# Kernel optimization log

Measured on AMD Instinct MI355X. Metric: run time of the kernel, lower is better.

The kernel has to match this reference:

```python
import jax, jax.numpy as jnp
import numpy as np

D = 768      # hidden size (hardcoded in module)
H = 8        # MHA heads
DH = D // H  # head dim = 96
SLOPE = 0.01 # LeakyReLU default negative slope
NEG = -1e9


def _leaky(x):
    return jnp.where(x >= 0, x, SLOPE * x)


def setup_inputs() -> dict:
    key = jax.random.key(0)
    ks = jax.random.split(key, 20)
    B, S, T, C, L = 32, 2048, 64, 512, 16
    seq = jax.random.normal(ks[0], (B, S, D), dtype=jnp.float32)
    tab_ids = jax.random.randint(ks[1], (B, T, L), 0, S, dtype=jnp.int32)
    col_ids = jax.random.randint(ks[2], (B, C, L), 0, S, dtype=jnp.int32)
    # contiguous column->table assignment (8 cols/table), mirrors cumulative
    # slicing by column_number_in_each_table and keeps every table non-empty
    t_of_c = jnp.broadcast_to(jnp.repeat(jnp.arange(T, dtype=jnp.int32), C // T), (B, C))
    g = lambda k, sh: (jax.random.normal(k, sh, dtype=jnp.float32) * 0.02)
    return {
        "sequence_embeddings": seq,
        "table_token_ids": tab_ids,
        "column_token_ids": col_ids,
        "table_of_column": t_of_c,
        "W_tab_pool": g(ks[3], (D, D)), "b_tab_pool": g(ks[4], (D,)),
        "W_col_pool": g(ks[5], (D, D)), "b_col_pool": g(ks[6], (D,)),
        "in_proj_w": g(ks[7], (3 * D, D)), "in_proj_b": g(ks[8], (3 * D,)),
        "out_proj_w": g(ks[9], (D, D)), "out_proj_b": g(ks[10], (D,)),
        "W_t1": g(ks[11], (D, 256)), "b_t1": g(ks[12], (256,)),
        "W_t2": g(ks[13], (256, 2)), "b_t2": g(ks[14], (2,)),
        "W_c1": g(ks[15], (D, 256)), "b_c1": g(ks[16], (256,)),
        "W_c2": g(ks[17], (256, 2)), "b_c2": g(ks[18], (2,)),
    }


def reference(sequence_embeddings, table_token_ids, column_token_ids, table_of_column,
              W_tab_pool, b_tab_pool, W_col_pool, b_col_pool,
              in_proj_w, in_proj_b, out_proj_w, out_proj_b,
              W_t1, b_t1, W_t2, b_t2, W_c1, b_c1, W_c2, b_c2):
    B, T = table_token_ids.shape[:2]
    C = column_token_ids.shape[1]
    bi = jnp.arange(B)[:, None, None]
    # ragged span sum-pooling (gather + segment sum)
    tab = sequence_embeddings[bi, table_token_ids].sum(axis=2)   # [B,T,D]
    col = sequence_embeddings[bi, column_token_ids].sum(axis=2)  # [B,C,D]
    tab = _leaky(tab @ W_tab_pool + b_tab_pool)
    col = _leaky(col @ W_col_pool + b_col_pool)
    # per-table cross-attention (table query over its own columns), batched + masked
    Wq, Wk, Wv = jnp.split(in_proj_w, 3, axis=0)
    bq, bk, bv = jnp.split(in_proj_b, 3, axis=0)
    q = (tab @ Wq.T + bq).reshape(B, T, H, DH)
    k = (col @ Wk.T + bk).reshape(B, C, H, DH)
    v = (col @ Wv.T + bv).reshape(B, C, H, DH)
    scores = jnp.einsum('bthd,bchd->bhtc', q, k) / jnp.sqrt(jnp.float32(DH))
    mask = table_of_column[:, None, None, :] == jnp.arange(T, dtype=table_of_column.dtype)[None, None, :, None]
    attn = jax.nn.softmax(jnp.where(mask, scores, NEG), axis=-1)
    ctx = jnp.einsum('bhtc,bchd->bthd', attn, v).reshape(B, T, D)
    tab = tab + (ctx @ out_proj_w.T + out_proj_b)
    tab = tab / jnp.maximum(jnp.linalg.norm(tab, axis=-1, keepdims=True), 1e-12)
    # classification heads (dropout in eval mode = identity)
    t_logits = _leaky(tab @ W_t1 + b_t1) @ W_t2 + b_t2  # [B,T,2]
    c_logits = _leaky(col @ W_c1 + b_c1) @ W_c2 + b_c2  # [B,C,2]
    return jnp.concatenate([t_logits, c_logits], axis=1)  # [B,T+C,2]
```

## Files before the change

kernel.cpp:

```cpp
#include <hip/hip_runtime.h>
#include <hip/hip_bf16.h>

constexpr int Bc = 32;
constexpr int Sc = 2048;
constexpr int Tc = 64;
constexpr int Cc = 512;
constexpr int Lc = 16;
constexpr int Dc = 768;
constexpr int Hc = 8;
constexpr int DHc = 96;

typedef __attribute__((ext_vector_type(4))) float f32x4;
typedef __attribute__((ext_vector_type(8))) short bf16x8;
typedef __hip_bfloat16 bf;

__device__ inline unsigned short f2bf(float f) {
  __hip_bfloat16 h = __float2bfloat16(f);
  return *reinterpret_cast<unsigned short*>(&h);
}
__device__ inline float us2f(unsigned short u) {
  return __uint_as_float(((unsigned)u) << 16);
}

#define GLDS16(gp, lp)                                                        \
  __builtin_amdgcn_global_load_lds(                                           \
      (const __attribute__((address_space(1))) void*)(gp),                    \
      (__attribute__((address_space(3))) void*)(lp), 16, 0, 0)

__device__ inline void transpose32(const float* __restrict__ in,
                                   bf* __restrict__ outp, int K, int N,
                                   int ti, float (*t)[33]) {
  int nx = N >> 5;
  int bx = (ti % nx) * 32, by = (ti / nx) * 32;
  int x = threadIdx.x & 31, y = threadIdx.x >> 5;
#pragma unroll
  for (int i = 0; i < 32; i += 8)
    t[y + i][x] = in[(size_t)(by + y + i) * N + bx + x];
  __syncthreads();
#pragma unroll
  for (int i = 0; i < 32; i += 8)
    outp[(size_t)(bx + y + i) * K + by + x] = __float2bfloat16(t[x][y + i]);
}

__global__ __launch_bounds__(256) void prep_kernel(
    const float* __restrict__ W_tab_pool, const float* __restrict__ W_col_pool,
    const float* __restrict__ W_t1, const float* __restrict__ W_c1,
    const float* __restrict__ in_proj_w, const float* __restrict__ out_proj_w,
    const float* __restrict__ b_t2, const float* __restrict__ b_c2,
    const float* __restrict__ seq, const int* __restrict__ t_of_c,
    bf* __restrict__ wtab_t, bf* __restrict__ wcol_t, bf* __restrict__ wt1_t,
    bf* __restrict__ wc1_t, bf* __restrict__ winproj, bf* __restrict__ woutproj,
    float* __restrict__ outd, ushort* __restrict__ seqb,
    int* __restrict__ col_sorted, int* __restrict__ offs) {
  __shared__ float t[32][33];
  __shared__ int cnt[Tc];
  __shared__ int cur[Tc + 1];
  int blk = blockIdx.x, tid = threadIdx.x;
  if (blk < 576) {
    transpose32(W_tab_pool, wtab_t, Dc, Dc, blk, t);
  } else if (blk < 1152) {
    transpose32(W_col_pool, wcol_t, Dc, Dc, blk - 576, t);
  } else if (blk < 1344) {
    transpose32(W_t1, wt1_t, Dc, 256, blk - 1152, t);
  } else if (blk < 1536) {
    transpose32(W_c1, wc1_t, Dc, 256, blk - 1344, t);
  } else if (blk < 3264) {
    int i = (blk - 1536) * 256 + tid;
    float4 v = reinterpret_cast<const float4*>(in_proj_w)[i];
    reinterpret_cast<ushort4*>(winproj)[i] =
        make_ushort4(f2bf(v.x), f2bf(v.y), f2bf(v.z), f2bf(v.w));
  } else if (blk < 3840) {
    int i = (blk - 3264) * 256 + tid;
    float4 v = reinterpret_cast<const float4*>(out_proj_w)[i];
    reinterpret_cast<ushort4*>(woutproj)[i] =
        make_ushort4(f2bf(v.x), f2bf(v.y), f2bf(v.z), f2bf(v.w));
  } else if (blk < 3984) {
    int e = (blk - 3840) * 256 + tid;
    int i = e & 1;
    int r = (e >> 1) % (Tc + Cc);
    outd[e] = (r < Tc) ? b_t2[i] : b_c2[i];
  } else if (blk < 28560) {
    int i0 = (blk - 3984) * 512 + tid;
    const float4* s4 = reinterpret_cast<const float4*>(seq);
    ushort4* o4 = reinterpret_cast<ushort4*>(seqb);
    float4 v = s4[i0];
    o4[i0] = make_ushort4(f2bf(v.x), f2bf(v.y), f2bf(v.z), f2bf(v.w));
    float4 v2 = s4[i0 + 256];
    o4[i0 + 256] = make_ushort4(f2bf(v2.x), f2bf(v2.y), f2bf(v2.z), f2bf(v2.w));
  } else {
    int b = blk - 28560;
    if (tid < Tc) cnt[tid] = 0;
    __syncthreads();
    for (int c = tid; c < Cc; c += 256) atomicAdd(&cnt[t_of_c[b * Cc + c]], 1);
    __syncthreads();
    if (tid == 0) {
      int off = 0;
      for (int tt = 0; tt < Tc; ++tt) {
        cur[tt] = off;
        off += cnt[tt];
      }
      cur[Tc] = off;
    }
    __syncthreads();
    if (tid <= Tc) offs[b * (Tc + 1) + tid] = cur[tid];
    __syncthreads();
    for (int c = tid; c < Cc; c += 256) {
      int tt = t_of_c[b * Cc + c];
      int pos = atomicAdd(&cur[tt], 1);
      col_sorted[b * Cc + pos] = c;
    }
  }
}

__global__ __launch_bounds__(256) void pool_kernel(
    const ushort* __restrict__ seqb, const int* __restrict__ tab_ids,
    const int* __restrict__ col_ids, ushort* __restrict__ tabp,
    ushort* __restrict__ colp) {
  int swz = (blockIdx.x & 7) * 576 + (blockIdx.x >> 3);
  int w = threadIdx.x >> 6, l = threadIdx.x & 63;
  int row = swz * 4 + w;
  int b = row / (Tc + Cc), r = row % (Tc + Cc);
  const int* ids;
  ushort* outp;
  if (r < Tc) {
    ids = tab_ids + ((size_t)b * Tc + r) * Lc;
    outp = tabp + ((size_t)b * Tc + r) * Dc;
  } else {
    int c = r - Tc;
    ids = col_ids + ((size_t)b * Cc + c) * Lc;
    outp = colp + ((size_t)b * Cc + c) * Dc;
  }
  float a0[4] = {0, 0, 0, 0}, a1[4] = {0, 0, 0, 0}, a2[4] = {0, 0, 0, 0};
#pragma unroll
  for (int tix = 0; tix < Lc; ++tix) {
    const ushort4* p =
        reinterpret_cast<const ushort4*>(seqb + ((size_t)b * Sc + ids[tix]) * Dc);
    ushort4 u0 = p[l], u1 = p[l + 64], u2 = p[l + 128];
    a0[0] += us2f(u0.x); a0[1] += us2f(u0.y); a0[2] += us2f(u0.z); a0[3] += us2f(u0.w);
    a1[0] += us2f(u1.x); a1[1] += us2f(u1.y); a1[2] += us2f(u1.z); a1[3] += us2f(u1.w);
    a2[0] += us2f(u2.x); a2[1] += us2f(u2.y); a2[2] += us2f(u2.z); a2[3] += us2f(u2.w);
  }
  ushort4* ob = reinterpret_cast<ushort4*>(outp);
  ob[l] = make_ushort4(f2bf(a0[0]), f2bf(a0[1]), f2bf(a0[2]), f2bf(a0[3]));
  ob[l + 64] = make_ushort4(f2bf(a1[0]), f2bf(a1[1]), f2bf(a1[2]), f2bf(a1[3]));
  ob[l + 128] = make_ushort4(f2bf(a2[0]), f2bf(a2[1]), f2bf(a2[2]), f2bf(a2[3]));
}

__device__ __forceinline__ void gemm_core(
    const bf* __restrict__ A, const bf* __restrict__ Bt,
    const float* __restrict__ bias, bf* __restrict__ Obf,
    float* __restrict__ Of32, const float* __restrict__ w2,
    float* __restrict__ outd, int out_base, int log2rpb, int bx, int by, int N,
    int leaky, int outmode) {
  constexpr int BM = 128, BN = 128, BK = 64, K = Dc;
  __shared__ bf As[BM * BK];
  __shared__ bf Bs[BN * BK];
  int tid = threadIdx.x;
  int row0 = by * BM, col0 = bx * BN;
  int w = tid >> 6, l = tid & 63;
  int wr = (w >> 1) * 64, wc = (w & 1) * 64;
  f32x4 acc[4][4];
#pragma unroll
  for (int m = 0; m < 4; ++m)
#pragma unroll
    for (int n = 0; n < 4; ++n) acc[m][n] = f32x4{0.f, 0.f, 0.f, 0.f};

  int srow = tid >> 3, skk = (tid & 7) * 8;
  const bf* gA = A + (size_t)(row0 + srow) * K + skk;
  const bf* gB = Bt + (size_t)(col0 + srow) * K + skk;
  char* lA = (char*)As + tid * 16;
  char* lB = (char*)Bs + tid * 16;
  int lr = l & 15, lk = (l >> 4) * 8;

  for (int k0 = 0; k0 < K; k0 += BK) {
#pragma unroll
    for (int c = 0; c < 4; ++c) {
      GLDS16(gA + k0 + (size_t)c * 32 * K, lA + c * 4096);
      GLDS16(gB + k0 + (size_t)c * 32 * K, lB + c * 4096);
    }
    __syncthreads();
    bf16x8 af[2][4], bfr[2][4];
#pragma unroll
    for (int ks = 0; ks < 2; ++ks) {
#pragma unroll
      for (int m = 0; m < 4; ++m)
        af[ks][m] = *reinterpret_cast<const bf16x8*>(
            &As[(wr + m * 16 + lr) * BK + ks * 32 + lk]);
#pragma unroll
      for (int n = 0; n < 4; ++n)
        bfr[ks][n] = *reinterpret_cast<const bf16x8*>(
            &Bs[(wc + n * 16 + lr) * BK + ks * 32 + lk]);
    }
#pragma unroll
    for (int ks = 0; ks < 2; ++ks)
#pragma unroll
      for (int m = 0; m < 4; ++m)
#pragma unroll
        for (int n = 0; n < 4; ++n)
          acc[m][n] = __builtin_amdgcn_mfma_f32_16x16x32_bf16(
              af[ks][m], bfr[ks][n], acc[m][n], 0, 0, 0);
    __syncthreads();
  }

  int colI = l & 15, rowb = (l >> 4) * 4;
  if (outmode == 3) {
    float w20[4], w21[4], bv[4];
#pragma unroll
    for (int n = 0; n < 4; ++n) {
      int c = col0 + wc + n * 16 + colI;
      w20[n] = w2[c * 2];
      w21[n] = w2[c * 2 + 1];
      bv[n] = bias[c];
    }
    float p0[4][4], p1[4][4];
#pragma unroll
    for (int m = 0; m < 4; ++m)
#pragma unroll
      for (int j = 0; j < 4; ++j) { p0[m][j] = 0.f; p1[m][j] = 0.f; }
#pragma unroll
    for (int m = 0; m < 4; ++m)
#pragma unroll
      for (int n = 0; n < 4; ++n)
#pragma unroll
        for (int j = 0; j < 4; ++j) {
          float v = acc[m][n][j] + bv[n];
          v = v >= 0.f ? v : 0.01f * v;
          p0[m][j] += v * w20[n];
          p1[m][j] += v * w21[n];
        }
#pragma unroll
    for (int m = 0; m < 4; ++m)
#pragma unroll
      for (int j = 0; j < 4; ++j) {
#pragma unroll
        for (int msk = 1; msk <= 8; msk <<= 1) {
          p0[m][j] += __shfl_xor(p0[m][j], msk);
          p1[m][j] += __shfl_xor(p1[m][j], msk);
        }
      }
    if (colI == 0) {
#pragma unroll
      for (int m = 0; m < 4; ++m)
#pragma unroll
        for (int j = 0; j < 4; ++j) {
          int grow = row0 + wr + m * 16 + rowb + j;
          int bb = grow >> log2rpb;
          int rr = grow & ((1 << log2rpb) - 1);
          int orow = bb * (Tc + Cc) + out_base + rr;
          atomicAdd(&outd[(size_t)orow * 2], p0[m][j]);
          atomicAdd(&outd[(size_t)orow * 2 + 1], p1[m][j]);
        }
    }
    return;
  }
#pragma unroll
  for (int m = 0; m < 4; ++m) {
#pragma unroll
    for (int n = 0; n < 4; ++n) {
      int c = col0 + wc + n * 16 + colI;
      float bv = bias ? bias[c] : 0.f;
#pragma unroll
      for (int j = 0; j < 4; ++j) {
        int r = row0 + wr + m * 16 + rowb + j;
        float v = acc[m][n][j] + bv;
        if (leaky) v = v >= 0.f ? v : 0.01f * v;
        if (outmode == 0 || outmode == 2) Obf[(size_t)r * N + c] = __float2bfloat16(v);
        if (outmode == 1 || outmode == 2) Of32[(size_t)r * N + c] = v;
      }
    }
  }
}

__global__ __launch_bounds__(256) void gemm_pools(
    const bf* __restrict__ tabp, const bf* __restrict__ colp,
    const bf* __restrict__ wtab_t, const bf* __restrict__ wcol_t,
    const float* __restrict__ b_tab, const float* __restrict__ b_col,
    bf* __restrict__ tabb_bf, float* __restrict__ tabb_f,
    bf* __restrict__ colb) {
  int id = (blockIdx.x & 7) * 108 + (blockIdx.x >> 3);
  if (id < 96) {
    gemm_core(tabp, wtab_t, b_tab, tabb_bf, tabb_f, nullptr, nullptr, 0, 0,
              id % 6, id / 6, Dc, 1, 2);
  } else {
    int r = id - 96;
    gemm_core(colp, wcol_t, b_col, colb, nullptr, nullptr, nullptr, 0, 0,
              r % 6, r / 6, Dc, 1, 0);
  }
}

__global__ __launch_bounds__(256) void gemm_qkvc(
    const bf* __restrict__ tabb_bf, const bf* __restrict__ colb,
    const bf* __restrict__ winproj, const float* __restrict__ in_proj_b,
    const bf* __restrict__ wc1_t, const float* __restrict__ b_c1,
    const float* __restrict__ W_c2, bf* __restrict__ qb, bf* __restrict__ kvb,
    float* __restrict__ outd) {
  int id = (blockIdx.x & 7) * 236 + (blockIdx.x >> 3);
  if (id < 96) {
    gemm_core(tabb_bf, winproj, in_proj_b, qb, nullptr, nullptr, nullptr, 0, 0,
              id % 6, id / 6, Dc, 0, 0);
  } else if (id < 1632) {
    int r = id - 96;
    gemm_core(colb, winproj + (size_t)Dc * Dc, in_proj_b + Dc, kvb, nullptr,
              nullptr, nullptr, 0, 0, r % 12, r / 12, 1536, 0, 0);
  } else {
    int r = id - 1632;
    gemm_core(colb, wc1_t, b_c1, nullptr, nullptr, W_c2, outd, Tc, 9, r % 2,
              r / 2, 256, 1, 3);
  }
}

__global__ __launch_bounds__(256) void gemm_single(
    const bf* __restrict__ A, const bf* __restrict__ Bt,
    const float* __restrict__ bias, bf* __restrict__ Obf,
    float* __restrict__ Of32, const float* __restrict__ w2,
    float* __restrict__ outd, int out_base, int log2rpb, int nbx, int N,
    int leaky, int outmode) {
  int chunk = gridDim.x >> 3;
  int id = (blockIdx.x & 7) * chunk + (blockIdx.x >> 3);
  gemm_core(A, Bt, bias, Obf, Of32, w2, outd, out_base, log2rpb, id % nbx,
            id / nbx, N, leaky, outmode);
}

__global__ __launch_bounds__(256) void attn_kernel(
    const bf* __restrict__ q, const bf* __restrict__ kv,
    const int* __restrict__ col_sorted, const int* __restrict__ offs,
    bf* __restrict__ ctx) {
  int b = blockIdx.x / Tc;
  int t = blockIdx.x % Tc;
  __shared__ float pbuf[Hc][Cc];
  __shared__ float den[Hc];
  __shared__ int cols_s[Cc];
  int tid = threadIdx.x;
  int o0 = offs[b * (Tc + 1) + t];
  int n = offs[b * (Tc + 1) + t + 1] - o0;
  for (int i = tid; i < n; i += 256)
    cols_s[i] = col_sorted[(size_t)b * Cc + o0 + i];
  __syncthreads();
  int h = tid >> 5, l32 = tid & 31, g = l32 >> 3, i8 = l32 & 7;
  const float scale = 0.10206207261596577f;
  float q12[12];
  {
    const ushort* qp =
        (const ushort*)q + ((size_t)b * Tc + t) * Dc + h * DHc + i8 * 12;
    ushort4 u0 = *(const ushort4*)(qp);
    ushort4 u1 = *(const ushort4*)(qp + 4);
    ushort4 u2 = *(const ushort4*)(qp + 8);
    q12[0] = us2f(u0.x); q12[1] = us2f(u0.y); q12[2] = us2f(u0.z); q12[3] = us2f(u0.w);
    q12[4] = us2f(u1.x); q12[5] = us2f(u1.y); q12[6] = us2f(u1.z); q12[7] = us2f(u1.w);
    q12[8] = us2f(u2.x); q12[9] = us2f(u2.y); q12[10] = us2f(u2.z); q12[11] = us2f(u2.w);
  }
  if (n > 0) {
    for (int jb = 0; jb < n; jb += 4) {
      int j = jb + g;
      float s = 0.f;
      if (j < n) {
        const ushort* kp = (const ushort*)kv +
                           ((size_t)b * Cc + cols_s[j]) * 1536 + h * DHc + i8 * 12;
        ushort4 u0 = *(const ushort4*)(kp);
        ushort4 u1 = *(const ushort4*)(kp + 4);
        ushort4 u2 = *(const ushort4*)(kp + 8);
        s += q12[0] * us2f(u0.x) + q12[1] * us2f(u0.y) + q12[2] * us2f(u0.z) +
             q12[3] * us2f(u0.w);
        s += q12[4] * us2f(u1.x) + q12[5] * us2f(u1.y) + q12[6] * us2f(u1.z) +
             q12[7] * us2f(u1.w);
        s += q12[8] * us2f(u2.x) + q12[9] * us2f(u2.y) + q12[10] * us2f(u2.z) +
             q12[11] * us2f(u2.w);
      }
      s += __shfl_xor(s, 1);
      s += __shfl_xor(s, 2);
      s += __shfl_xor(s, 4);
      if (j < n && i8 == 0) pbuf[h][j] = s * scale;
    }
  }
  __syncthreads();
  if (n > 0) {
    float lmax = -3.0e38f;
    for (int j = l32; j < n; j += 32) lmax = fmaxf(lmax, pbuf[h][j]);
#pragma unroll
    for (int m = 16; m >= 1; m >>= 1) lmax = fmaxf(lmax, __shfl_xor(lmax, m));
    float lsum = 0.f;
    for (int j = l32; j < n; j += 32) {
      float e = __expf(pbuf[h][j] - lmax);
      pbuf[h][j] = e;
      lsum += e;
    }
#pragma unroll
    for (int m = 16; m >= 1; m >>= 1) lsum += __shfl_xor(lsum, m);
    if (l32 == 0) den[h] = lsum;
  } else if (l32 == 0) {
    den[h] = (float)Cc;
  }
  __syncthreads();
  int ncols = n > 0 ? n : Cc;
  float a12[12];
#pragma unroll
  for (int d = 0; d < 12; ++d) a12[d] = 0.f;
  for (int jb = 0; jb < ncols; jb += 4) {
    int j = jb + g;
    if (j < ncols) {
      int cj = n > 0 ? cols_s[j] : j;
      float pw = n > 0 ? pbuf[h][j] : 1.f;
      const ushort* vp = (const ushort*)kv + ((size_t)b * Cc + cj) * 1536 +
                         768 + h * DHc + i8 * 12;
      ushort4 u0 = *(const ushort4*)(vp);
      ushort4 u1 = *(const ushort4*)(vp + 4);
      ushort4 u2 = *(const ushort4*)(vp + 8);
      a12[0] += pw * us2f(u0.x); a12[1] += pw * us2f(u0.y);
      a12[2] += pw * us2f(u0.z); a12[3] += pw * us2f(u0.w);
      a12[4] += pw * us2f(u1.x); a12[5] += pw * us2f(u1.y);
      a12[6] += pw * us2f(u1.z); a12[7] += pw * us2f(u1.w);
      a12[8] += pw * us2f(u2.x); a12[9] += pw * us2f(u2.y);
      a12[10] += pw * us2f(u2.z); a12[11] += pw * us2f(u2.w);
    }
  }
#pragma unroll
  for (int d = 0; d < 12; ++d) {
    a12[d] += __shfl_xor(a12[d], 8);
    a12[d] += __shfl_xor(a12[d], 16);
  }
  float inv = 1.0f / den[h];
  if (g == 0) {
    ushort* cp = (ushort*)ctx + ((size_t)b * Tc + t) * Dc + h * DHc + i8 * 12;
    *(ushort4*)(cp) = make_ushort4(f2bf(a12[0] * inv), f2bf(a12[1] * inv),
                                   f2bf(a12[2] * inv), f2bf(a12[3] * inv));
    *(ushort4*)(cp + 4) = make_ushort4(f2bf(a12[4] * inv), f2bf(a12[5] * inv),
                                       f2bf(a12[6] * inv), f2bf(a12[7] * inv));
    *(ushort4*)(cp + 8) = make_ushort4(f2bf(a12[8] * inv), f2bf(a12[9] * inv),
                                       f2bf(a12[10] * inv), f2bf(a12[11] * inv));
  }
}

__global__ __launch_bounds__(256) void addnorm_kernel(
    const float* __restrict__ tab, const float* __restrict__ proj,
    bf* __restrict__ tabn) {
  int row = blockIdx.x;
  int tid = threadIdx.x;
  size_t base = (size_t)row * Dc;
  float x0 = tab[base + tid] + proj[base + tid];
  float x1 = tab[base + tid + 256] + proj[base + tid + 256];
  float x2 = tab[base + tid + 512] + proj[base + tid + 512];
  float ss = x0 * x0 + x1 * x1 + x2 * x2;
#pragma unroll
  for (int m = 32; m >= 1; m >>= 1) ss += __shfl_xor(ss, m);
  __shared__ float red[4];
  int wave = tid >> 6, lane = tid & 63;
  if (lane == 0) red[wave] = ss;
  __syncthreads();
  float total = red[0] + red[1] + red[2] + red[3];
  float sc = 1.0f / fmaxf(sqrtf(total), 1e-12f);
  tabn[base + tid] = __float2bfloat16(x0 * sc);
  tabn[base + tid + 256] = __float2bfloat16(x1 * sc);
  tabn[base + tid + 512] = __float2bfloat16(x2 * sc);
}

extern "C" void kernel_launch(void* const* d_in, const int* in_sizes, int n_in,
                              void* d_out, int out_size, void* d_ws,
                              size_t ws_size, hipStream_t stream) {
  const float* seq = (const float*)d_in[0];
  const int* tab_ids = (const int*)d_in[1];
  const int* col_ids = (const int*)d_in[2];
  const int* t_of_c = (const int*)d_in[3];
  const float* W_tab_pool = (const float*)d_in[4];
  const float* b_tab_pool = (const float*)d_in[5];
  const float* W_col_pool = (const float*)d_in[6];
  const float* b_col_pool = (const float*)d_in[7];
  const float* in_proj_w = (const float*)d_in[8];
  const float* in_proj_b = (const float*)d_in[9];
  const float* out_proj_w = (const float*)d_in[10];
  const float* out_proj_b = (const float*)d_in[11];
  const float* W_t1 = (const float*)d_in[12];
  const float* b_t1 = (const float*)d_in[13];
  const float* W_t2 = (const float*)d_in[14];
  const float* b_t2 = (const float*)d_in[15];
  const float* W_c1 = (const float*)d_in[16];
  const float* b_c1 = (const float*)d_in[17];
  const float* W_c2 = (const float*)d_in[18];
  const float* b_c2 = (const float*)d_in[19];
  float* out = (float*)d_out;

  char* p = (char*)d_ws;
  auto alloc = [&](size_t bytes) -> char* {
    char* r = p;
    p += (bytes + 255) & ~(size_t)255;
    return r;
  };
  const size_t nBT = (size_t)Bc * Tc;
  const size_t nBC = (size_t)Bc * Cc;
  ushort* seqb = (ushort*)alloc((size_t)Bc * Sc * Dc * 2);
  bf* tabp = (bf*)alloc(nBT * Dc * 2);
  bf* colp = (bf*)alloc(nBC * Dc * 2);
  bf* tabb_bf = (bf*)alloc(nBT * Dc * 2);
  float* tabb_f = (float*)alloc(nBT * Dc * 4);
  bf* colb = (bf*)alloc(nBC * Dc * 2);
  bf* qb = (bf*)alloc(nBT * Dc * 2);
  bf* kvb = (bf*)alloc(nBC * 1536 * 2);
  bf* ctxb = (bf*)alloc(nBT * Dc * 2);
  float* projb = (float*)alloc(nBT * Dc * 4);
  bf* tabn = (bf*)alloc(nBT * Dc * 2);
  bf* wtab_t = (bf*)alloc((size_t)Dc * Dc * 2);
  bf* wcol_t = (bf*)alloc((size_t)Dc * Dc * 2);
  bf* winproj = (bf*)alloc((size_t)3 * Dc * Dc * 2);
  bf* woutproj = (bf*)alloc((size_t)Dc * Dc * 2);
  bf* wt1_t = (bf*)alloc((size_t)256 * Dc * 2);
  bf* wc1_t = (bf*)alloc((size_t)256 * Dc * 2);
  int* col_sorted = (int*)alloc(nBC * 4);
  int* offs = (int*)alloc((size_t)Bc * (Tc + 1) * 4);

  prep_kernel<<<28592, 256, 0, stream>>>(
      W_tab_pool, W_col_pool, W_t1, W_c1, in_proj_w, out_proj_w, b_t2, b_c2,
      seq, t_of_c, wtab_t, wcol_t, wt1_t, wc1_t, winproj, woutproj, out,
      seqb, col_sorted, offs);
  pool_kernel<<<Bc * (Tc + Cc) / 4, 256, 0, stream>>>(seqb, tab_ids, col_ids,
                                                      (ushort*)tabp,
                                                      (ushort*)colp);
  gemm_pools<<<864, 256, 0, stream>>>(tabp, colp, wtab_t, wcol_t, b_tab_pool,
                                      b_col_pool, tabb_bf, tabb_f, colb);
  gemm_qkvc<<<1888, 256, 0, stream>>>(tabb_bf, colb, winproj, in_proj_b, wc1_t,
                                      b_c1, W_c2, qb, kvb, out);
  attn_kernel<<<Bc * Tc, 256, 0, stream>>>(qb, kvb, col_sorted, offs, ctxb);
  gemm_single<<<96, 256, 0, stream>>>(ctxb, woutproj, out_proj_b, nullptr,
                                      projb, nullptr, nullptr, 0, 0, 6, Dc, 0,
                                      1);
  addnorm_kernel<<<nBT, 256, 0, stream>>>(tabb_f, projb, tabn);
  gemm_single<<<32, 256, 0, stream>>>(tabn, wt1_t, b_t1, nullptr, nullptr,
                                      W_t2, out, 0, 6, 2, 256, 1, 3);
}
```

Measured before the change: 572.1 us.

## Double-buffer GEMM LDS, fuse residual+norm into out-proj epilogue, rebalance kernels

The shared GEMM core now uses double-buffered LDS tiles, so the next K slice is prefetched while the current one feeds the MFMA instructions, and one barrier per iteration is dropped. The separate add-and-normalize kernel is removed. The out-projection epilogue now adds the residual, writes bf16, and accumulates per-row sums of squares with atomics. The final t1 head applies the 1/norm scale inside its epilogue. The column classification head moves from the QKV launch into the out-projection launch, which removes one launch and one fp32 round trip, at the cost of doubled LDS per block (lower occupancy) and atomic-order nondeterminism.

```diff
diff --git a/kernel.cpp b/kernel.cpp
--- a/kernel.cpp
+++ b/kernel.cpp
@@ -51,7 +51,8 @@
     bf* __restrict__ wtab_t, bf* __restrict__ wcol_t, bf* __restrict__ wt1_t,
     bf* __restrict__ wc1_t, bf* __restrict__ winproj, bf* __restrict__ woutproj,
     float* __restrict__ outd, ushort* __restrict__ seqb,
-    int* __restrict__ col_sorted, int* __restrict__ offs) {
+    int* __restrict__ col_sorted, int* __restrict__ offs,
+    float* __restrict__ ssq) {
   __shared__ float t[32][33];
   __shared__ int cnt[Tc];
   __shared__ int cur[Tc + 1];
@@ -87,7 +88,7 @@
     o4[i0] = make_ushort4(f2bf(v.x), f2bf(v.y), f2bf(v.z), f2bf(v.w));
     float4 v2 = s4[i0 + 256];
     o4[i0 + 256] = make_ushort4(f2bf(v2.x), f2bf(v2.y), f2bf(v2.z), f2bf(v2.w));
-  } else {
+  } else if (blk < 28592) {
     int b = blk - 28560;
     if (tid < Tc) cnt[tid] = 0;
     __syncthreads();
@@ -109,6 +110,9 @@
       int pos = atomicAdd(&cur[tt], 1);
       col_sorted[b * Cc + pos] = c;
     }
+  } else {
+#pragma unroll
+    for (int i = 0; i < 8; ++i) ssq[tid * 8 + i] = 0.f;
   }
 }
 
@@ -150,11 +154,13 @@
     const bf* __restrict__ A, const bf* __restrict__ Bt,
     const float* __restrict__ bias, bf* __restrict__ Obf,
     float* __restrict__ Of32, const float* __restrict__ w2,
-    float* __restrict__ outd, int out_base, int log2rpb, int bx, int by, int N,
-    int leaky, int outmode) {
+    float* __restrict__ outd, int out_base, int log2rpb,
+    const float* __restrict__ tabf, float* __restrict__ ssq,
+    const float* __restrict__ ssrd, int bx, int by, int N, int leaky,
+    int outmode) {
   constexpr int BM = 128, BN = 128, BK = 64, K = Dc;
-  __shared__ bf As[BM * BK];
-  __shared__ bf Bs[BN * BK];
+  __shared__ bf As[2][BM * BK];
+  __shared__ bf Bs[2][BN * BK];
   int tid = threadIdx.x;
   int row0 = by * BM, col0 = bx * BN;
   int w = tid >> 6, l = tid & 63;
@@ -168,28 +174,37 @@
   int srow = tid >> 3, skk = (tid & 7) * 8;
   const bf* gA = A + (size_t)(row0 + srow) * K + skk;
   const bf* gB = Bt + (size_t)(col0 + srow) * K + skk;
-  char* lA = (char*)As + tid * 16;
-  char* lB = (char*)Bs + tid * 16;
+  char* lA = (char*)&As[0][0] + tid * 16;
+  char* lB = (char*)&Bs[0][0] + tid * 16;
   int lr = l & 15, lk = (l >> 4) * 8;
 
+#pragma unroll
+  for (int c = 0; c < 4; ++c) {
+    GLDS16(gA + (size_t)c * 32 * K, lA + c * 4096);
+    GLDS16(gB + (size_t)c * 32 * K, lB + c * 4096);
+  }
+  __syncthreads();
+  int cur = 0;
   for (int k0 = 0; k0 < K; k0 += BK) {
-#pragma unroll
-    for (int c = 0; c < 4; ++c) {
-      GLDS16(gA + k0 + (size_t)c * 32 * K, lA + c * 4096);
-      GLDS16(gB + k0 + (size_t)c * 32 * K, lB + c * 4096);
-    }
-    __syncthreads();
+    if (k0 + BK < K) {
+      int nb = cur ^ 1;
+#pragma unroll
+      for (int c = 0; c < 4; ++c) {
+        GLDS16(gA + k0 + BK + (size_t)c * 32 * K, lA + nb * 16384 + c * 4096);
+        GLDS16(gB + k0 + BK + (size_t)c * 32 * K, lB + nb * 16384 + c * 4096);
+      }
+    }
     bf16x8 af[2][4], bfr[2][4];
 #pragma unroll
     for (int ks = 0; ks < 2; ++ks) {
 #pragma unroll
       for (int m = 0; m < 4; ++m)
         af[ks][m] = *reinterpret_cast<const bf16x8*>(
-            &As[(wr + m * 16 + lr) * BK + ks * 32 + lk]);
+            &As[cur][(wr + m * 16 + lr) * BK + ks * 32 + lk]);
 #pragma unroll
       for (int n = 0; n < 4; ++n)
         bfr[ks][n] = *reinterpret_cast<const bf16x8*>(
-            &Bs[(wc + n * 16 + lr) * BK + ks * 32 + lk]);
+            &Bs[cur][(wc + n * 16 + lr) * BK + ks * 32 + lk]);
     }
 #pragma unroll
     for (int ks = 0; ks < 2; ++ks)
@@ -199,7 +214,8 @@
         for (int n = 0; n < 4; ++n)
           acc[m][n] = __builtin_amdgcn_mfma_f32_16x16x32_bf16(
               af[ks][m], bfr[ks][n], acc[m][n], 0, 0, 0);
-    __syncthreads();
+    if (k0 + BK < K) __syncthreads();
+    cur ^= 1;
   }
 
   int colI = l & 15, rowb = (l >> 4) * 4;
@@ -212,6 +228,18 @@
       w21[n] = w2[c * 2 + 1];
       bv[n] = bias[c];
     }
+    float scr[4][4];
+#pragma unroll
+    for (int m = 0; m < 4; ++m)
+#pragma unroll
+      for (int j = 0; j < 4; ++j) {
+        if (ssrd) {
+          int r = row0 + wr + m * 16 + rowb + j;
+          scr[m][j] = 1.f / fmaxf(sqrtf(ssrd[r]), 1e-12f);
+        } else {
+          scr[m][j] = 1.f;
+        }
+      }
     float p0[4][4], p1[4][4];
 #pragma unroll
     for (int m = 0; m < 4; ++m)
@@ -223,7 +251,7 @@
       for (int n = 0; n < 4; ++n)
 #pragma unroll
         for (int j = 0; j < 4; ++j) {
-          float v = acc[m][n][j] + bv[n];
+          float v = scr[m][j] * acc[m][n][j] + bv[n];
           v = v >= 0.f ? v : 0.01f * v;
           p0[m][j] += v * w20[n];
           p1[m][j] += v * w21[n];
@@ -253,6 +281,43 @@
     }
     return;
   }
+  if (outmode == 4) {
+    float sq[4][4];
+#pragma unroll
+    for (int m = 0; m < 4; ++m)
+#pragma unroll
+      for (int j = 0; j < 4; ++j) sq[m][j] = 0.f;
+#pragma unroll
+    for (int m = 0; m < 4; ++m)
+#pragma unroll
+      for (int n = 0; n < 4; ++n) {
+        int c = col0 + wc + n * 16 + colI;
+        float bv = bias[c];
+#pragma unroll
+        for (int j = 0; j < 4; ++j) {
+          int r = row0 + wr + m * 16 + rowb + j;
+          float x = acc[m][n][j] + bv + tabf[(size_t)r * N + c];
+          Obf[(size_t)r * N + c] = __float2bfloat16(x);
+          sq[m][j] += x * x;
+        }
+      }
+#pragma unroll
+    for (int m = 0; m < 4; ++m)
+#pragma unroll
+      for (int j = 0; j < 4; ++j) {
+#pragma unroll
+        for (int msk = 1; msk <= 8; msk <<= 1)
+          sq[m][j] += __shfl_xor(sq[m][j], msk);
+      }
+    if (colI == 0) {
+#pragma unroll
+      for (int m = 0; m < 4; ++m)
+#pragma unroll
+        for (int j = 0; j < 4; ++j)
+          atomicAdd(&ssq[row0 + wr + m * 16 + rowb + j], sq[m][j]);
+    }
+    return;
+  }
 #pragma unroll
   for (int m = 0; m < 4; ++m) {
 #pragma unroll
@@ -264,8 +329,8 @@
         int r = row0 + wr + m * 16 + rowb + j;
         float v = acc[m][n][j] + bv;
         if (leaky) v = v >= 0.f ? v : 0.01f * v;
-        if (outmode == 0 || outmode == 2) Obf[(size_t)r * N + c] = __float2bfloat16(v);
-        if (outmode == 1 || outmode == 2) Of32[(size_t)r * N + c] = v;
+        Obf[(size_t)r * N + c] = __float2bfloat16(v);
+        if (outmode == 2 && Of32) Of32[(size_t)r * N + c] = v;
       }
     }
   }
@@ -278,47 +343,63 @@
     bf* __restrict__ tabb_bf, float* __restrict__ tabb_f,
     bf* __restrict__ colb) {
   int id = (blockIdx.x & 7) * 108 + (blockIdx.x >> 3);
+  const bf* Aa; const bf* Bb; const float* bb; bf* Oo; float* Ff;
+  int bx, by;
   if (id < 96) {
-    gemm_core(tabp, wtab_t, b_tab, tabb_bf, tabb_f, nullptr, nullptr, 0, 0,
-              id % 6, id / 6, Dc, 1, 2);
+    Aa = tabp; Bb = wtab_t; bb = b_tab; Oo = tabb_bf; Ff = tabb_f;
+    bx = id % 6; by = id / 6;
   } else {
     int r = id - 96;
-    gemm_core(colp, wcol_t, b_col, colb, nullptr, nullptr, nullptr, 0, 0,
-              r % 6, r / 6, Dc, 1, 0);
-  }
-}
-
-__global__ __launch_bounds__(256) void gemm_qkvc(
+    Aa = colp; Bb = wcol_t; bb = b_col; Oo = colb; Ff = nullptr;
+    bx = r % 6; by = r / 6;
+  }
+  gemm_core(Aa, Bb, bb, Oo, Ff, nullptr, nullptr, 0, 0, nullptr, nullptr,
+            nullptr, bx, by, Dc, 1, 2);
+}
+
+__global__ __launch_bounds__(256) void gemm_qkv(
     const bf* __restrict__ tabb_bf, const bf* __restrict__ colb,
     const bf* __restrict__ winproj, const float* __restrict__ in_proj_b,
+    bf* __restrict__ qb, bf* __restrict__ kvb) {
+  int id = (blockIdx.x & 7) * 204 + (blockIdx.x >> 3);
+  const bf* Aa; const bf* Bb; const float* bb; bf* Oo;
+  int bx, by, NN;
+  if (id < 96) {
+    Aa = tabb_bf; Bb = winproj; bb = in_proj_b; Oo = qb;
+    bx = id % 6; by = id / 6; NN = Dc;
+  } else {
+    int r = id - 96;
+    Aa = colb; Bb = winproj + (size_t)Dc * Dc; bb = in_proj_b + Dc; Oo = kvb;
+    bx = r % 12; by = r / 12; NN = 1536;
+  }
+  gemm_core(Aa, Bb, bb, Oo, nullptr, nullptr, nullptr, 0, 0, nullptr, nullptr,
+            nullptr, bx, by, NN, 0, 0);
+}
+
+__global__ __launch_bounds__(256) void gemm_oc(
+    const bf* __restrict__ ctxb, const bf* __restrict__ woutproj,
+    const float* __restrict__ out_proj_b, const float* __restrict__ tabb_f,
+    bf* __restrict__ xbf, float* __restrict__ ssq, const bf* __restrict__ colb,
     const bf* __restrict__ wc1_t, const float* __restrict__ b_c1,
-    const float* __restrict__ W_c2, bf* __restrict__ qb, bf* __restrict__ kvb,
-    float* __restrict__ outd) {
-  int id = (blockIdx.x & 7) * 236 + (blockIdx.x >> 3);
+    const float* __restrict__ W_c2, float* __restrict__ outd) {
+  int id = (blockIdx.x & 7) * 44 + (blockIdx.x >> 3);
   if (id < 96) {
-    gemm_core(tabb_bf, winproj, in_proj_b, qb, nullptr, nullptr, nullptr, 0, 0,
-              id % 6, id / 6, Dc, 0, 0);
-  } else if (id < 1632) {
+    gemm_core(ctxb, woutproj, out_proj_b, xbf, nullptr, nullptr, nullptr, 0, 0,
+              tabb_f, ssq, nullptr, id % 6, id / 6, Dc, 0, 4);
+  } else {
     int r = id - 96;
-    gemm_core(colb, winproj + (size_t)Dc * Dc, in_proj_b + Dc, kvb, nullptr,
-              nullptr, nullptr, 0, 0, r % 12, r / 12, 1536, 0, 0);
-  } else {
-    int r = id - 1632;
-    gemm_core(colb, wc1_t, b_c1, nullptr, nullptr, W_c2, outd, Tc, 9, r % 2,
-              r / 2, 256, 1, 3);
-  }
-}
-
-__global__ __launch_bounds__(256) void gemm_single(
-    const bf* __restrict__ A, const bf* __restrict__ Bt,
-    const float* __restrict__ bias, bf* __restrict__ Obf,
-    float* __restrict__ Of32, const float* __restrict__ w2,
-    float* __restrict__ outd, int out_base, int log2rpb, int nbx, int N,
-    int leaky, int outmode) {
-  int chunk = gridDim.x >> 3;
-  int id = (blockIdx.x & 7) * chunk + (blockIdx.x >> 3);
-  gemm_core(A, Bt, bias, Obf, Of32, w2, outd, out_base, log2rpb, id % nbx,
-            id / nbx, N, leaky, outmode);
+    gemm_core(colb, wc1_t, b_c1, nullptr, nullptr, W_c2, outd, Tc, 9, nullptr,
+              nullptr, nullptr, r % 2, r / 2, 256, 1, 3);
+  }
+}
+
+__global__ __launch_bounds__(256) void gemm_t1(
+    const bf* __restrict__ xbf, const bf* __restrict__ wt1_t,
+    const float* __restrict__ b_t1, const float* __restrict__ W_t2,
+    const float* __restrict__ ssq, float* __restrict__ outd) {
+  int id = (blockIdx.x & 7) * 4 + (blockIdx.x >> 3);
+  gemm_core(xbf, wt1_t, b_t1, nullptr, nullptr, W_t2, outd, 0, 6, nullptr,
+            nullptr, ssq, id % 2, id / 2, 256, 1, 3);
 }
 
 __global__ __launch_bounds__(256) void attn_kernel(
@@ -430,29 +511,6 @@
   }
 }
 
-__global__ __launch_bounds__(256) void addnorm_kernel(
-    const float* __restrict__ tab, const float* __restrict__ proj,
-    bf* __restrict__ tabn) {
-  int row = blockIdx.x;
-  int tid = threadIdx.x;
-  size_t base = (size_t)row * Dc;
-  float x0 = tab[base + tid] + proj[base + tid];
-  float x1 = tab[base + tid + 256] + proj[base + tid + 256];
-  float x2 = tab[base + tid + 512] + proj[base + tid + 512];
-  float ss = x0 * x0 + x1 * x1 + x2 * x2;
-#pragma unroll
-  for (int m = 32; m >= 1; m >>= 1) ss += __shfl_xor(ss, m);
-  __shared__ float red[4];
-  int wave = tid >> 6, lane = tid & 63;
-  if (lane == 0) red[wave] = ss;
-  __syncthreads();
-  float total = red[0] + red[1] + red[2] + red[3];
-  float sc = 1.0f / fmaxf(sqrtf(total), 1e-12f);
-  tabn[base + tid] = __float2bfloat16(x0 * sc);
-  tabn[base + tid + 256] = __float2bfloat16(x1 * sc);
-  tabn[base + tid + 512] = __float2bfloat16(x2 * sc);
-}
-
 extern "C" void kernel_launch(void* const* d_in, const int* in_sizes, int n_in,
                               void* d_out, int out_size, void* d_ws,
                               size_t ws_size, hipStream_t stream) {
@@ -495,8 +553,8 @@
   bf* qb = (bf*)alloc(nBT * Dc * 2);
   bf* kvb = (bf*)alloc(nBC * 1536 * 2);
   bf* ctxb = (bf*)alloc(nBT * Dc * 2);
-  float* projb = (float*)alloc(nBT * Dc * 4);
-  bf* tabn = (bf*)alloc(nBT * Dc * 2);
+  bf* xbf = (bf*)alloc(nBT * Dc * 2);
+  float* ssq = (float*)alloc(nBT * 4);
   bf* wtab_t = (bf*)alloc((size_t)Dc * Dc * 2);
   bf* wcol_t = (bf*)alloc((size_t)Dc * Dc * 2);
   bf* winproj = (bf*)alloc((size_t)3 * Dc * Dc * 2);
@@ -506,22 +564,19 @@
   int* col_sorted = (int*)alloc(nBC * 4);
   int* offs = (int*)alloc((size_t)Bc * (Tc + 1) * 4);
 
-  prep_kernel<<<28592, 256, 0, stream>>>(
+  prep_kernel<<<28593, 256, 0, stream>>>(
       W_tab_pool, W_col_pool, W_t1, W_c1, in_proj_w, out_proj_w, b_t2, b_c2,
-      seq, t_of_c, wtab_t, wcol_t, wt1_t, wc1_t, winproj, woutproj, out,
-      seqb, col_sorted, offs);
+      seq, t_of_c, wtab_t, wcol_t, wt1_t, wc1_t, winproj, woutproj, out, seqb,
+      col_sorted, offs, ssq);
   pool_kernel<<<Bc * (Tc + Cc) / 4, 256, 0, stream>>>(seqb, tab_ids, col_ids,
                                                       (ushort*)tabp,
                                                       (ushort*)colp);
   gemm_pools<<<864, 256, 0, stream>>>(tabp, colp, wtab_t, wcol_t, b_tab_pool,
                                       b_col_pool, tabb_bf, tabb_f, colb);
-  gemm_qkvc<<<1888, 256, 0, stream>>>(tabb_bf, colb, winproj, in_proj_b, wc1_t,
-                                      b_c1, W_c2, qb, kvb, out);
+  gemm_qkv<<<1632, 256, 0, stream>>>(tabb_bf, colb, winproj, in_proj_b, qb,
+                                     kvb);
   attn_kernel<<<Bc * Tc, 256, 0, stream>>>(qb, kvb, col_sorted, offs, ctxb);
-  gemm_single<<<96, 256, 0, stream>>>(ctxb, woutproj, out_proj_b, nullptr,
-                                      projb, nullptr, nullptr, 0, 0, 6, Dc, 0,
-                                      1);
-  addnorm_kernel<<<nBT, 256, 0, stream>>>(tabb_f, projb, tabn);
-  gemm_single<<<32, 256, 0, stream>>>(tabn, wt1_t, b_t1, nullptr, nullptr,
-                                      W_t2, out, 0, 6, 2, 256, 1, 3);
-}
+  gemm_oc<<<352, 256, 0, stream>>>(ctxb, woutproj, out_proj_b, tabb_f, xbf,
+                                   ssq, colb, wc1_t, b_c1, W_c2, out);
+  gemm_t1<<<32, 256, 0, stream>>>(xbf, wt1_t, b_t1, W_t2, ssq, out);
+}
```

Result: no change. 577.3 us (+0.9%).
